# Kernel tuning notes

Measured on AMD Instinct MI355X. Metric: run time of the kernel, lower is better.

The kernel has to match this reference:

```python
import jax, jax.numpy as jnp
import numpy as np

CLIP = 16          # relative_clip
REL = 2 * CLIP + 1 # relative_size = 33
NEG = 1e9


def setup_inputs() -> dict:
    key = jax.random.key(0)
    k1, k2, k3, k4, k5 = jax.random.split(key, 5)
    B, L, D = 8, 2048, 64
    return {
        "query": jax.random.normal(k1, (B, L, D), jnp.float32),
        "key": jax.random.normal(k2, (B, L, D), jnp.float32),
        "value": jax.random.normal(k3, (B, L, D), jnp.float32),
        "mask": jnp.ones((B, 1, L), jnp.float32),
        "key_relative": jax.random.normal(k4, (REL, D), jnp.float32),
        "value_relative": jax.random.normal(k5, (REL, D), jnp.float32),
    }


def reference(query, key, value, mask, key_relative, value_relative):
    B, Q, Dk = query.shape
    K = key.shape[1]
    scale = jnp.asarray(np.sqrt(Dk), query.dtype)

    # dot products [B,Q,K] (torch code does broadcast-mul+sum; matmul is same math)
    dot = jnp.einsum('bqd,bkd->bqk', query, key)

    # relative key bias: dot_relative [B,Q,REL], gathered by diag_id[q,k]
    dot_rel = jnp.einsum('bqd,td->bqt', query, key_relative)
    qi = jnp.arange(Q)[:, None]
    kj = jnp.arange(K)[None, :]
    diag_id = jnp.clip(qi - kj + CLIP, 0, 2 * CLIP)           # [Q,K]
    rel_bias = jnp.take_along_axis(
        dot_rel, jnp.broadcast_to(diag_id[None], (B, Q, K)), axis=2)
    dot = dot + rel_bias

    # only_attend_front: causal mask (strict upper triangle penalized)
    causal = jnp.triu(jnp.ones((K, K), dot.dtype), 1) * NEG   # [K,K]
    dot = dot - causal[None]

    # padding mask (broadcast)
    dot = dot - (1.0 - mask) * NEG

    logits = dot / scale
    probs = jax.nn.softmax(logits, axis=-1)
    # zero rows where every position is masked out
    n_masked = jnp.sum(dot <= -5e8, axis=-1, keepdims=True)
    probs = probs * (n_masked < K).astype(probs.dtype)
    # dropout with droprate=0.0 / eval mode -> identity

    res = jnp.einsum('bqk,bkd->bqd', probs, value)

    # relative value recombination: recover_id[q,r] = q + r - CLIP, OOB -> K (zero col)
    recover = jnp.arange(Q)[:, None] + jnp.arange(REL)[None, :] - CLIP  # [Q,REL]
    recover = jnp.where((recover < 0) | (recover >= K), K, recover)
    probs_pad = jnp.concatenate(
        [probs, jnp.zeros((B, Q, 1), probs.dtype)], axis=-1)           # [B,Q,K+1]
    rel_probs = jnp.take_along_axis(
        probs_pad, jnp.broadcast_to(recover[None], (B, Q, REL)), axis=2)
    res = res + jnp.einsum('bqr,rd->bqd', rel_probs, value_relative)
    return res
```

## Files before the change

kernel.cpp:

```cpp
#include <hip/hip_runtime.h>

typedef __attribute__((ext_vector_type(4))) float f32x4;
typedef __attribute__((ext_vector_type(8))) short s16x8;
typedef __attribute__((ext_vector_type(4))) short s16x4;

#define LSEQ 2048
#define NB   8
#define CH   8
#define UPB  80
#define NUNIT 640

#define OFF_QB    0x000000u
#define OFF_KB    0x200000u
#define OFF_VTB   0x400000u
#define OFF_PEN   0x600000u
#define OFF_KREL  0x610000u
#define OFF_OPART 0x620000u
#define OFF_ML    0x1020000u

__device__ __forceinline__ unsigned short f2bf(float f) {
    union { float f; unsigned int u; } v; v.f = f;
    unsigned int u = v.u;
    return (unsigned short)((u + 0x7fffu + ((u >> 16) & 1u)) >> 16);
}

__device__ __forceinline__ float bf2f(unsigned short b) {
    union { unsigned int u; float f; } v; v.u = ((unsigned int)b) << 16;
    return v.f;
}

__global__ __launch_bounds__(256)
void convert_kernel(const float* __restrict__ Q, const float* __restrict__ K,
                    const float* __restrict__ V, const float* __restrict__ Msk,
                    const float* __restrict__ Krel, char* __restrict__ ws)
{
    const int tid = threadIdx.x;
    const int bid = blockIdx.x;
    unsigned short* Qb  = (unsigned short*)(ws + OFF_QB);
    unsigned short* Kb  = (unsigned short*)(ws + OFF_KB);
    unsigned short* VTb = (unsigned short*)(ws + OFF_VTB);
    float*          pen = (float*)(ws + OFF_PEN);
    unsigned short* Krb = (unsigned short*)(ws + OFF_KREL);

    if (bid < 1024) {
        int base = bid * 1024 + tid * 4;
        f32x4 q4 = *(const f32x4*)(Q + base);
        s16x4 o;
        o.x = (short)f2bf(q4.x * 0.125f); o.y = (short)f2bf(q4.y * 0.125f);
        o.z = (short)f2bf(q4.z * 0.125f); o.w = (short)f2bf(q4.w * 0.125f);
        *(s16x4*)(Qb + base) = o;
    } else if (bid < 2048) {
        int base = (bid - 1024) * 1024 + tid * 4;
        f32x4 k4 = *(const f32x4*)(K + base);
        s16x4 o;
        o.x = (short)f2bf(k4.x); o.y = (short)f2bf(k4.y);
        o.z = (short)f2bf(k4.z); o.w = (short)f2bf(k4.w);
        *(s16x4*)(Kb + base) = o;
    } else if (bid < 2304) {
        __shared__ unsigned short tileT[64][72];
        int tile = bid - 2048;
        int b = tile >> 5, k0 = (tile & 31) << 6;
        #pragma unroll
        for (int rep = 0; rep < 4; ++rep) {
            int idx = tid + rep * 256;
            int kr = idx >> 4, dc0 = (idx & 15) << 2;
            f32x4 v4 = *(const f32x4*)(V + (size_t)(b * 2048 + k0 + kr) * 64 + dc0);
            tileT[dc0 + 0][kr] = f2bf(v4.x);
            tileT[dc0 + 1][kr] = f2bf(v4.y);
            tileT[dc0 + 2][kr] = f2bf(v4.z);
            tileT[dc0 + 3][kr] = f2bf(v4.w);
        }
        __syncthreads();
        #pragma unroll
        for (int rep = 0; rep < 2; ++rep) {
            int idx = tid + rep * 256;
            int d = idx >> 3, ch = idx & 7;
            *(s16x8*)(VTb + (size_t)(b * 64 + d) * 2048 + k0 + ch * 8) =
                *(const s16x8*)&tileT[d][ch * 8];
        }
    } else if (bid < 2312) {
        int i0 = (bid - 2304) * 2048 + tid * 8;
        f32x4 m0 = *(const f32x4*)(Msk + i0);
        f32x4 m1 = *(const f32x4*)(Msk + i0 + 4);
        f32x4 p0 = (m0 - 1.0f) * 1.25e8f;
        f32x4 p1 = (m1 - 1.0f) * 1.25e8f;
        *(f32x4*)(pen + i0) = p0;
        *(f32x4*)(pen + i0 + 4) = p1;
    } else {
        for (int g = tid; g < 768; g += 256) {
            int e = g * 4, row = e >> 6, col = e & 63;
            s16x4 o;
            if (row < 33) {
                f32x4 v = *(const f32x4*)(Krel + row * 64 + col);
                o.x = (short)f2bf(v.x); o.y = (short)f2bf(v.y);
                o.z = (short)f2bf(v.z); o.w = (short)f2bf(v.w);
            } else {
                o.x = 0; o.y = 0; o.z = 0; o.w = 0;
            }
            *(s16x4*)(Krb + row * 64 + col) = o;
        }
    }
}

#define LDS_KS   0
#define LDS_VT   8192
#define LDS_P    16384
#define LDS_DREL 24576
#define LDS_VREL 29696
#define LDS_TOT  34592

__device__ __forceinline__ void near_bias(f32x4& sv, const f32x4& pv, int cc,
                                          int k0, int g0, int q,
                                          const float* drel) {
#pragma unroll
    for (int r = 0; r < 4; ++r) {
        int kk = k0 + cc * 16 + 4 * g0 + r;
        int dlt = q - kk;
        int idx = dlt < 16 ? dlt : 16;
        idx = idx < 0 ? 0 : idx;
        float bb = drel[idx];
        float v = sv[r] + bb + pv[r];
        sv[r] = (dlt < 0) ? -1e30f : v;
    }
}

__global__ __launch_bounds__(256, 3)
void attn_main(const float* __restrict__ Vrel_g, float* __restrict__ Out,
               char* __restrict__ ws)
{
    __shared__ __align__(16) char lds[LDS_TOT];
    const int tid  = threadIdx.x;
    const int wv   = tid >> 6;
    const int lane = tid & 63;
    const int g0   = lane >> 4;
    const int qh   = lane & 15;

    int u = blockIdx.x;
    int b = u / UPB;
    int u2 = u - b * UPB;
    int t, chunk, nck;
    if (u2 < 8)       { t = u2;               chunk = 0;          nck = 1; }
    else if (u2 < 24) { t = 8  + (u2 - 8) / 2;  chunk = (u2 - 8) & 1;  nck = 2; }
    else if (u2 < 48) { t = 16 + (u2 - 24) / 3; chunk = (u2 - 24) % 3; nck = 3; }
    else              { t = 24 + (u2 - 48) / 4; chunk = (u2 - 48) & 3; nck = 4; }
    const int q0   = t << 6;
    const int q0w  = q0 + wv * 16;
    const int q    = q0w + qh;
    const int ck0  = chunk * CH;
    const int ckend = min(ck0 + CH, t + 1);
    const bool is_final = (nck == 1);

    const unsigned short* Qb  = (const unsigned short*)(ws + OFF_QB);
    const unsigned short* Kb  = (const unsigned short*)(ws + OFF_KB);
    const unsigned short* VTb = (const unsigned short*)(ws + OFF_VTB);
    const float*          pen = (const float*)(ws + OFF_PEN);
    const unsigned short* Krb = (const unsigned short*)(ws + OFF_KREL);

    const size_t qrow = (size_t)(b * 2048 + q) * 64;
    s16x8 qf0 = *(const s16x8*)(Qb + qrow + 0 * 32 + g0 * 8);
    s16x8 qf1 = *(const s16x8*)(Qb + qrow + 1 * 32 + g0 * 8);

    {
        s16x8 a10 = *(const s16x8*)(Krb + (16 + qh) * 64 + 0 * 32 + g0 * 8);
        s16x8 a11 = *(const s16x8*)(Krb + (16 + qh) * 64 + 1 * 32 + g0 * 8);
        s16x8 a20 = *(const s16x8*)(Krb + (32 + qh) * 64 + 0 * 32 + g0 * 8);
        s16x8 a21 = *(const s16x8*)(Krb + (32 + qh) * 64 + 1 * 32 + g0 * 8);
        f32x4 z = {0.f, 0.f, 0.f, 0.f};
        f32x4 d1 = __builtin_amdgcn_mfma_f32_16x16x32_bf16(a10, qf0, z, 0, 0, 0);
        d1 = __builtin_amdgcn_mfma_f32_16x16x32_bf16(a11, qf1, d1, 0, 0, 0);
        f32x4 d2 = __builtin_amdgcn_mfma_f32_16x16x32_bf16(a20, qf0, z, 0, 0, 0);
        d2 = __builtin_amdgcn_mfma_f32_16x16x32_bf16(a21, qf1, d2, 0, 0, 0);
        float* drel = (float*)(lds + LDS_DREL) + wv * 320 + qh * 20;
        drel[4 * g0 + 0] = d1.x; drel[4 * g0 + 1] = d1.y;
        drel[4 * g0 + 2] = d1.z; drel[4 * g0 + 3] = d1.w;
        if (g0 == 0) drel[16] = d2.x;
    }
    asm volatile("" ::: "memory");
    const float* drelT = (const float*)(lds + LDS_DREL) + wv * 320 + qh * 20;
    float bias32 = drelT[16];

    {
        float* vr = (float*)(lds + LDS_VREL);
        for (int i = tid; i < 17 * 16; i += 256) {
            int row = i >> 4, c4 = (i & 15) << 2;
            *(f32x4*)(vr + row * 72 + c4) = *(const f32x4*)(Vrel_g + row * 64 + c4);
        }
    }

    f32x4 o0 = {0,0,0,0}, o1 = {0,0,0,0}, o2 = {0,0,0,0}, o3 = {0,0,0,0};
    float mprev = -1e30f, lsum = 0.f;

    char* KsL = lds + LDS_KS;
    char* VtL = lds + LDS_VT;
    char* PL  = lds + LDS_P + wv * 2048;
    const int swzq = (qh & 7) << 4;
    const float* vrel = (const float*)(lds + LDS_VREL);

    for (int kt = ck0; kt < ckend; ++kt) {
        const int k0 = kt << 6;
        __syncthreads();
        #pragma unroll
        for (int rep = 0; rep < 2; ++rep) {
            int idx = tid + rep * 256;
            int row = idx >> 3, cb = (idx & 7) << 4;
            int sw = cb ^ ((row & 7) << 4);
            *(s16x8*)(KsL + row * 128 + sw) =
                *(const s16x8*)((const char*)(Kb + (size_t)(b * 2048 + k0 + row) * 64) + cb);
            *(s16x8*)(VtL + row * 128 + sw) =
                *(const s16x8*)((const char*)(VTb + (size_t)(b * 64 + row) * 2048 + k0) + cb);
        }
        __syncthreads();

        if (k0 <= q0w + 15) {
            f32x4 s0, s1, s2, s3;
            {
                f32x4 z = {0,0,0,0};
                const int b0 = (16 * g0) ^ swzq;
                const int b1 = (64 + 16 * g0) ^ swzq;
                s16x8 a00 = *(const s16x8*)(KsL + (0  + qh) * 128 + b0);
                s16x8 a01 = *(const s16x8*)(KsL + (0  + qh) * 128 + b1);
                s16x8 a10 = *(const s16x8*)(KsL + (16 + qh) * 128 + b0);
                s16x8 a11 = *(const s16x8*)(KsL + (16 + qh) * 128 + b1);
                s16x8 a20 = *(const s16x8*)(KsL + (32 + qh) * 128 + b0);
                s16x8 a21 = *(const s16x8*)(KsL + (32 + qh) * 128 + b1);
                s16x8 a30 = *(const s16x8*)(KsL + (48 + qh) * 128 + b0);
                s16x8 a31 = *(const s16x8*)(KsL + (48 + qh) * 128 + b1);
                s0 = __builtin_amdgcn_mfma_f32_16x16x32_bf16(a00, qf0, z, 0, 0, 0);
                s0 = __builtin_amdgcn_mfma_f32_16x16x32_bf16(a01, qf1, s0, 0, 0, 0);
                s1 = __builtin_amdgcn_mfma_f32_16x16x32_bf16(a10, qf0, z, 0, 0, 0);
                s1 = __builtin_amdgcn_mfma_f32_16x16x32_bf16(a11, qf1, s1, 0, 0, 0);
                s2 = __builtin_amdgcn_mfma_f32_16x16x32_bf16(a20, qf0, z, 0, 0, 0);
                s2 = __builtin_amdgcn_mfma_f32_16x16x32_bf16(a21, qf1, s2, 0, 0, 0);
                s3 = __builtin_amdgcn_mfma_f32_16x16x32_bf16(a30, qf0, z, 0, 0, 0);
                s3 = __builtin_amdgcn_mfma_f32_16x16x32_bf16(a31, qf1, s3, 0, 0, 0);
            }
            const float* penb = pen + b * 2048 + k0 + 4 * g0;
            f32x4 pn0 = *(const f32x4*)(penb + 0);
            f32x4 pn1 = *(const f32x4*)(penb + 16);
            f32x4 pn2 = *(const f32x4*)(penb + 32);
            f32x4 pn3 = *(const f32x4*)(penb + 48);
            const bool near = (k0 + 79 >= q0w);
            if (!near) {
                s0 += pn0 + bias32; s1 += pn1 + bias32;
                s2 += pn2 + bias32; s3 += pn3 + bias32;
            } else {
                near_bias(s0, pn0, 0, k0, g0, q, drelT);
                near_bias(s1, pn1, 1, k0, g0, q, drelT);
                near_bias(s2, pn2, 2, k0, g0, q, drelT);
                near_bias(s3, pn3, 3, k0, g0, q, drelT);
            }
            float mt = fmaxf(fmaxf(fmaxf(s0.x, s0.y), fmaxf(s0.z, s0.w)),
                      fmaxf(fmaxf(fmaxf(s1.x, s1.y), fmaxf(s1.z, s1.w)),
                      fmaxf(fmaxf(fmaxf(s2.x, s2.y), fmaxf(s2.z, s2.w)),
                            fmaxf(fmaxf(s3.x, s3.y), fmaxf(s3.z, s3.w)))));
            mt = fmaxf(mt, __shfl_xor(mt, 16));
            mt = fmaxf(mt, __shfl_xor(mt, 32));
            float mnew = fmaxf(mprev, mt);
            float fsc = __expf(mprev - mnew);
            s0.x = __expf(s0.x - mnew); s0.y = __expf(s0.y - mnew);
            s0.z = __expf(s0.z - mnew); s0.w = __expf(s0.w - mnew);
            s1.x = __expf(s1.x - mnew); s1.y = __expf(s1.y - mnew);
            s1.z = __expf(s1.z - mnew); s1.w = __expf(s1.w - mnew);
            s2.x = __expf(s2.x - mnew); s2.y = __expf(s2.y - mnew);
            s2.z = __expf(s2.z - mnew); s2.w = __expf(s2.w - mnew);
            s3.x = __expf(s3.x - mnew); s3.y = __expf(s3.y - mnew);
            s3.z = __expf(s3.z - mnew); s3.w = __expf(s3.w - mnew);
            float rs = (s0.x + s0.y + s0.z + s0.w) + (s1.x + s1.y + s1.z + s1.w)
                     + (s2.x + s2.y + s2.z + s2.w) + (s3.x + s3.y + s3.z + s3.w);
            rs += __shfl_xor(rs, 16);
            rs += __shfl_xor(rs, 32);
            lsum = lsum * fsc + rs;
            mprev = mnew;
            o0 *= fsc; o1 *= fsc; o2 *= fsc; o3 *= fsc;

            {
                s16x4 pk;
                pk.x = (short)f2bf(s0.x); pk.y = (short)f2bf(s0.y);
                pk.z = (short)f2bf(s0.z); pk.w = (short)f2bf(s0.w);
                *(s16x4*)(PL + qh * 128 + ((0  + 8 * g0) ^ swzq)) = pk;
                pk.x = (short)f2bf(s1.x); pk.y = (short)f2bf(s1.y);
                pk.z = (short)f2bf(s1.z); pk.w = (short)f2bf(s1.w);
                *(s16x4*)(PL + qh * 128 + ((32 + 8 * g0) ^ swzq)) = pk;
                pk.x = (short)f2bf(s2.x); pk.y = (short)f2bf(s2.y);
                pk.z = (short)f2bf(s2.z); pk.w = (short)f2bf(s2.w);
                *(s16x4*)(PL + qh * 128 + ((64 + 8 * g0) ^ swzq)) = pk;
                pk.x = (short)f2bf(s3.x); pk.y = (short)f2bf(s3.y);
                pk.z = (short)f2bf(s3.z); pk.w = (short)f2bf(s3.w);
                *(s16x4*)(PL + qh * 128 + ((96 + 8 * g0) ^ swzq)) = pk;
            }
            asm volatile("" ::: "memory");
            {
                const int b0 = (16 * g0) ^ swzq;
                const int b1 = (64 + 16 * g0) ^ swzq;
                s16x8 bP0 = *(const s16x8*)(PL + qh * 128 + b0);
                s16x8 bP1 = *(const s16x8*)(PL + qh * 128 + b1);
                asm volatile("" ::: "memory");
                s16x8 v00 = *(const s16x8*)(VtL + (0  + qh) * 128 + b0);
                s16x8 v01 = *(const s16x8*)(VtL + (0  + qh) * 128 + b1);
                s16x8 v10 = *(const s16x8*)(VtL + (16 + qh) * 128 + b0);
                s16x8 v11 = *(const s16x8*)(VtL + (16 + qh) * 128 + b1);
                s16x8 v20 = *(const s16x8*)(VtL + (32 + qh) * 128 + b0);
                s16x8 v21 = *(const s16x8*)(VtL + (32 + qh) * 128 + b1);
                s16x8 v30 = *(const s16x8*)(VtL + (48 + qh) * 128 + b0);
                s16x8 v31 = *(const s16x8*)(VtL + (48 + qh) * 128 + b1);
                o0 = __builtin_amdgcn_mfma_f32_16x16x32_bf16(v00, bP0, o0, 0, 0, 0);
                o0 = __builtin_amdgcn_mfma_f32_16x16x32_bf16(v01, bP1, o0, 0, 0, 0);
                o1 = __builtin_amdgcn_mfma_f32_16x16x32_bf16(v10, bP0, o1, 0, 0, 0);
                o1 = __builtin_amdgcn_mfma_f32_16x16x32_bf16(v11, bP1, o1, 0, 0, 0);
                o2 = __builtin_amdgcn_mfma_f32_16x16x32_bf16(v20, bP0, o2, 0, 0, 0);
                o2 = __builtin_amdgcn_mfma_f32_16x16x32_bf16(v21, bP1, o2, 0, 0, 0);
                o3 = __builtin_amdgcn_mfma_f32_16x16x32_bf16(v30, bP0, o3, 0, 0, 0);
                o3 = __builtin_amdgcn_mfma_f32_16x16x32_bf16(v31, bP1, o3, 0, 0, 0);
            }
            if (near) {
                const int kql = q - k0;
                #pragma unroll
                for (int dlt = 0; dlt <= 16; ++dlt) {
                    int kkl = kql - dlt;
                    if (kkl >= 0 && kkl < 64) {
                        float p = bf2f(*(const unsigned short*)
                                       (PL + qh * 128 + ((2 * kkl) ^ swzq)));
                        const float* vrow = vrel + (16 - dlt) * 72 + 4 * g0;
                        o0 += p * *(const f32x4*)(vrow + 0);
                        o1 += p * *(const f32x4*)(vrow + 16);
                        o2 += p * *(const f32x4*)(vrow + 32);
                        o3 += p * *(const f32x4*)(vrow + 48);
                    }
                }
            }
        }
    }

    if (is_final) {
        float inv = 1.f / lsum;
        float* op = Out + (size_t)(b * 2048 + q) * 64 + 4 * g0;
        *(f32x4*)(op + 0)  = o0 * inv;
        *(f32x4*)(op + 16) = o1 * inv;
        *(f32x4*)(op + 32) = o2 * inv;
        *(f32x4*)(op + 48) = o3 * inv;
    } else {
        float* op = (float*)(ws + OFF_OPART) + (size_t)u * 4096 + (wv * 16 + qh) * 64 + 4 * g0;
        *(f32x4*)(op + 0)  = o0;
        *(f32x4*)(op + 16) = o1;
        *(f32x4*)(op + 32) = o2;
        *(f32x4*)(op + 48) = o3;
        if (g0 == 0) {
            float* ml = (float*)(ws + OFF_ML) + (size_t)u * 128 + (wv * 16 + qh) * 2;
            ml[0] = mprev; ml[1] = lsum;
        }
    }
}

__global__ __launch_bounds__(256)
void combine_kernel(float* __restrict__ Out, const char* __restrict__ ws)
{
    int bid = blockIdx.x;
    int b = bid / 24;
    int t = 8 + bid % 24;
    int nck = t / 8 + 1;
    int S;
    if (t < 16)      S = 8 + 2 * (t - 8);
    else if (t < 24) S = 24 + 3 * (t - 16);
    else             S = 48 + 4 * (t - 24);
    int ubase = b * UPB + S;
    int tid = threadIdx.x;
    int qloc = tid >> 2;
    int d0 = (tid & 3) << 4;
    const float* mlb = (const float*)(ws + OFF_ML);
    const float* opb = (const float*)(ws + OFF_OPART);

    float m[4], l[4];
    float M = -1e30f;
    #pragma unroll
    for (int i = 0; i < 4; ++i) {
        if (i < nck) {
            const float* ml = mlb + (size_t)(ubase + i) * 128 + qloc * 2;
            m[i] = ml[0]; l[i] = ml[1];
            M = fmaxf(M, m[i]);
        }
    }
    float L = 0.f;
    float coef[4];
    #pragma unroll
    for (int i = 0; i < 4; ++i) {
        if (i < nck) { coef[i] = __expf(m[i] - M); L += l[i] * coef[i]; }
    }
    f32x4 a0 = {0,0,0,0}, a1 = {0,0,0,0}, a2 = {0,0,0,0}, a3 = {0,0,0,0};
    #pragma unroll
    for (int i = 0; i < 4; ++i) {
        if (i < nck) {
            const float* op = opb + (size_t)(ubase + i) * 4096 + qloc * 64 + d0;
            a0 += coef[i] * *(const f32x4*)(op + 0);
            a1 += coef[i] * *(const f32x4*)(op + 4);
            a2 += coef[i] * *(const f32x4*)(op + 8);
            a3 += coef[i] * *(const f32x4*)(op + 12);
        }
    }
    float inv = 1.f / L;
    float* oo = Out + (size_t)(b * 2048 + t * 64 + qloc) * 64 + d0;
    *(f32x4*)(oo + 0)  = a0 * inv;
    *(f32x4*)(oo + 4)  = a1 * inv;
    *(f32x4*)(oo + 8)  = a2 * inv;
    *(f32x4*)(oo + 12) = a3 * inv;
}

extern "C" void kernel_launch(void* const* d_in, const int* in_sizes, int n_in,
                              void* d_out, int out_size, void* d_ws, size_t ws_size,
                              hipStream_t stream) {
    (void)in_sizes; (void)n_in; (void)out_size; (void)ws_size;
    const float* Q    = (const float*)d_in[0];
    const float* K    = (const float*)d_in[1];
    const float* V    = (const float*)d_in[2];
    const float* Msk  = (const float*)d_in[3];
    const float* Krel = (const float*)d_in[4];
    const float* Vrel = (const float*)d_in[5];
    float* Out = (float*)d_out;
    char* ws = (char*)d_ws;

    convert_kernel<<<2313, 256, 0, stream>>>(Q, K, V, Msk, Krel, ws);
    attn_main<<<NUNIT, 256, 0, stream>>>(Vrel, Out, ws);
    combine_kernel<<<192, 256, 0, stream>>>(Out, ws);
}
```

Baseline: 103.5 us.

## Double-buffer K/V tiles via register prefetch and fold log2e into exp2 softmax

The main loop now prefetches the next K and V^T tile into registers before the barrier and writes them into a second LDS buffer after the current tile's compute. This cuts the per-iteration barriers from two to one and overlaps global loads with MFMA and softmax work. The query and padding-penalty scales also absorb log2(e), so the softmax and the combine step can use the native exp2 instruction instead of __expf. The cost is a larger LDS footprint per block, which may limit how many blocks fit on each CU, plus extra live registers.

```diff
diff --git a/kernel.cpp b/kernel.cpp
--- a/kernel.cpp
+++ b/kernel.cpp
@@ -9,6 +9,9 @@
 #define CH   8
 #define UPB  80
 #define NUNIT 640
+
+#define QSCALE   0.180336880f
+#define PENSCALE 1.8033688e8f
 
 #define OFF_QB    0x000000u
 #define OFF_KB    0x200000u
@@ -46,8 +49,8 @@
         int base = bid * 1024 + tid * 4;
         f32x4 q4 = *(const f32x4*)(Q + base);
         s16x4 o;
-        o.x = (short)f2bf(q4.x * 0.125f); o.y = (short)f2bf(q4.y * 0.125f);
-        o.z = (short)f2bf(q4.z * 0.125f); o.w = (short)f2bf(q4.w * 0.125f);
+        o.x = (short)f2bf(q4.x * QSCALE); o.y = (short)f2bf(q4.y * QSCALE);
+        o.z = (short)f2bf(q4.z * QSCALE); o.w = (short)f2bf(q4.w * QSCALE);
         *(s16x4*)(Qb + base) = o;
     } else if (bid < 2048) {
         int base = (bid - 1024) * 1024 + tid * 4;
@@ -82,8 +85,8 @@
         int i0 = (bid - 2304) * 2048 + tid * 8;
         f32x4 m0 = *(const f32x4*)(Msk + i0);
         f32x4 m1 = *(const f32x4*)(Msk + i0 + 4);
-        f32x4 p0 = (m0 - 1.0f) * 1.25e8f;
-        f32x4 p1 = (m1 - 1.0f) * 1.25e8f;
+        f32x4 p0 = (m0 - 1.0f) * PENSCALE;
+        f32x4 p1 = (m1 - 1.0f) * PENSCALE;
         *(f32x4*)(pen + i0) = p0;
         *(f32x4*)(pen + i0 + 4) = p1;
     } else {
@@ -102,12 +105,12 @@
     }
 }
 
-#define LDS_KS   0
-#define LDS_VT   8192
-#define LDS_P    16384
-#define LDS_DREL 24576
-#define LDS_VREL 29696
-#define LDS_TOT  34592
+#define LDS_BUF0 0
+#define LDS_BUF1 16384
+#define LDS_P    32768
+#define LDS_DREL 40960
+#define LDS_VREL 46080
+#define LDS_TOT  50976
 
 __device__ __forceinline__ void near_bias(f32x4& sv, const f32x4& pv, int cc,
                                           int k0, int g0, int q,
@@ -190,26 +193,50 @@
     f32x4 o0 = {0,0,0,0}, o1 = {0,0,0,0}, o2 = {0,0,0,0}, o3 = {0,0,0,0};
     float mprev = -1e30f, lsum = 0.f;
 
-    char* KsL = lds + LDS_KS;
-    char* VtL = lds + LDS_VT;
     char* PL  = lds + LDS_P + wv * 2048;
     const int swzq = (qh & 7) << 4;
     const float* vrel = (const float*)(lds + LDS_VREL);
 
-    for (int kt = ck0; kt < ckend; ++kt) {
+    const int idx0 = tid,        idx1 = tid + 256;
+    const int row0 = idx0 >> 3,  cb0 = (idx0 & 7) << 4;
+    const int row1 = idx1 >> 3,  cb1 = (idx1 & 7) << 4;
+    const int sw0 = cb0 ^ ((row0 & 7) << 4);
+    const int sw1 = cb1 ^ ((row1 & 7) << 4);
+    const char* ksrc0 = (const char*)(Kb  + (size_t)(b * 2048 + row0) * 64) + cb0;
+    const char* ksrc1 = (const char*)(Kb  + (size_t)(b * 2048 + row1) * 64) + cb1;
+    const char* vsrc0 = (const char*)(VTb + (size_t)(b * 64 + row0) * 2048) + cb0;
+    const char* vsrc1 = (const char*)(VTb + (size_t)(b * 64 + row1) * 2048) + cb1;
+
+    s16x8 rk0, rk1, rv0, rv1;
+#define LOADREGS(KT)                                                          \
+    do {                                                                      \
+        rk0 = *(const s16x8*)(ksrc0 + (size_t)(KT) * 8192);                   \
+        rk1 = *(const s16x8*)(ksrc1 + (size_t)(KT) * 8192);                   \
+        rv0 = *(const s16x8*)(vsrc0 + (size_t)(KT) * 128);                    \
+        rv1 = *(const s16x8*)(vsrc1 + (size_t)(KT) * 128);                    \
+    } while (0)
+#define STOREREGS(BASE)                                                       \
+    do {                                                                      \
+        *(s16x8*)((BASE) + row0 * 128 + sw0) = rk0;                           \
+        *(s16x8*)((BASE) + row1 * 128 + sw1) = rk1;                           \
+        *(s16x8*)((BASE) + 8192 + row0 * 128 + sw0) = rv0;                    \
+        *(s16x8*)((BASE) + 8192 + row1 * 128 + sw1) = rv1;                    \
+    } while (0)
+
+    LOADREGS(ck0);
+    STOREREGS(lds + LDS_BUF0);
+
+    const int nkt = ckend - ck0;
+    for (int it = 0; it < nkt; ++it) {
+        const int kt = ck0 + it;
         const int k0 = kt << 6;
+        const int cur = it & 1;
+        const bool havenext = (it + 1 < nkt);
+        if (havenext) LOADREGS(kt + 1);
         __syncthreads();
-        #pragma unroll
-        for (int rep = 0; rep < 2; ++rep) {
-            int idx = tid + rep * 256;
-            int row = idx >> 3, cb = (idx & 7) << 4;
-            int sw = cb ^ ((row & 7) << 4);
-            *(s16x8*)(KsL + row * 128 + sw) =
-                *(const s16x8*)((const char*)(Kb + (size_t)(b * 2048 + k0 + row) * 64) + cb);
-            *(s16x8*)(VtL + row * 128 + sw) =
-                *(const s16x8*)((const char*)(VTb + (size_t)(b * 64 + row) * 2048 + k0) + cb);
-        }
-        __syncthreads();
+
+        char* KsL = lds + (cur ? LDS_BUF1 : LDS_BUF0);
+        char* VtL = KsL + 8192;
 
         if (k0 <= q0w + 15) {
             f32x4 s0, s1, s2, s3;
@@ -256,15 +283,15 @@
             mt = fmaxf(mt, __shfl_xor(mt, 16));
             mt = fmaxf(mt, __shfl_xor(mt, 32));
             float mnew = fmaxf(mprev, mt);
-            float fsc = __expf(mprev - mnew);
-            s0.x = __expf(s0.x - mnew); s0.y = __expf(s0.y - mnew);
-            s0.z = __expf(s0.z - mnew); s0.w = __expf(s0.w - mnew);
-            s1.x = __expf(s1.x - mnew); s1.y = __expf(s1.y - mnew);
-            s1.z = __expf(s1.z - mnew); s1.w = __expf(s1.w - mnew);
-            s2.x = __expf(s2.x - mnew); s2.y = __expf(s2.y - mnew);
-            s2.z = __expf(s2.z - mnew); s2.w = __expf(s2.w - mnew);
-            s3.x = __expf(s3.x - mnew); s3.y = __expf(s3.y - mnew);
-            s3.z = __expf(s3.z - mnew); s3.w = __expf(s3.w - mnew);
+            float fsc = __builtin_amdgcn_exp2f(mprev - mnew);
+            s0.x = __builtin_amdgcn_exp2f(s0.x - mnew); s0.y = __builtin_amdgcn_exp2f(s0.y - mnew);
+            s0.z = __builtin_amdgcn_exp2f(s0.z - mnew); s0.w = __builtin_amdgcn_exp2f(s0.w - mnew);
+            s1.x = __builtin_amdgcn_exp2f(s1.x - mnew); s1.y = __builtin_amdgcn_exp2f(s1.y - mnew);
+            s1.z = __builtin_amdgcn_exp2f(s1.z - mnew); s1.w = __builtin_amdgcn_exp2f(s1.w - mnew);
+            s2.x = __builtin_amdgcn_exp2f(s2.x - mnew); s2.y = __builtin_amdgcn_exp2f(s2.y - mnew);
+            s2.z = __builtin_amdgcn_exp2f(s2.z - mnew); s2.w = __builtin_amdgcn_exp2f(s2.w - mnew);
+            s3.x = __builtin_amdgcn_exp2f(s3.x - mnew); s3.y = __builtin_amdgcn_exp2f(s3.y - mnew);
+            s3.z = __builtin_amdgcn_exp2f(s3.z - mnew); s3.w = __builtin_amdgcn_exp2f(s3.w - mnew);
             float rs = (s0.x + s0.y + s0.z + s0.w) + (s1.x + s1.y + s1.z + s1.w)
                      + (s2.x + s2.y + s2.z + s2.w) + (s3.x + s3.y + s3.z + s3.w);
             rs += __shfl_xor(rs, 16);
@@ -329,6 +356,10 @@
                 }
             }
         }
+
+        if (havenext) {
+            STOREREGS(lds + ((cur ^ 1) ? LDS_BUF1 : LDS_BUF0));
+        }
     }
 
     if (is_final) {
@@ -383,7 +414,7 @@
     float coef[4];
     #pragma unroll
     for (int i = 0; i < 4; ++i) {
-        if (i < nck) { coef[i] = __expf(m[i] - M); L += l[i] * coef[i]; }
+        if (i < nck) { coef[i] = __builtin_amdgcn_exp2f(m[i] - M); L += l[i] * coef[i]; }
     }
     f32x4 a0 = {0,0,0,0}, a1 = {0,0,0,0}, a2 = {0,0,0,0}, a3 = {0,0,0,0};
     #pragma unroll
```

Result: no change. 102.8 us (-0.7%).
